# Kernel optimization log

Hardware: AMD Instinct MI355X
Metric: run time of the kernel (lower is better)

The kernel has to match this reference:

```python
import jax, jax.numpy as jnp
import numpy as np

B, L, C = 2, 2048, 1024
H, DK = 16, 64  # multiNum, dk
EPS = 1e-5
MASK_VAL = -2**15 + 1  # matches masked_fill value in torch source


def layer_norm(x, g, b):
    mu = jnp.mean(x, axis=-1, keepdims=True)
    var = jnp.var(x, axis=-1, keepdims=True)
    return (x - mu) * jax.lax.rsqrt(var + EPS) * g + b


def setup_inputs() -> dict:
    key = jax.random.key(0)
    ks = jax.random.split(key, 12)
    s_in = 1.0 / np.sqrt(C)
    s_attn = 1.0 / np.sqrt(H * DK)
    return {
        "qx": jax.random.normal(ks[0], (B, L, C), jnp.float32),
        "kx": jax.random.normal(ks[1], (B, L, C), jnp.float32),
        "vx": jax.random.normal(ks[2], (B, L, C), jnp.float32),
        "maskPAD": jax.random.randint(ks[3], (B, L, L), 0, 2, jnp.int32),
        "ln_g": jnp.ones((C,), jnp.float32),
        "ln_b": jnp.zeros((C,), jnp.float32),
        "wq": jax.random.uniform(ks[4], (C, H * DK), jnp.float32, -s_in, s_in),
        "bq": jax.random.uniform(ks[5], (H * DK,), jnp.float32, -s_in, s_in),
        "wk": jax.random.uniform(ks[6], (C, H * DK), jnp.float32, -s_in, s_in),
        "bk": jax.random.uniform(ks[7], (H * DK,), jnp.float32, -s_in, s_in),
        "wv": jax.random.uniform(ks[8], (C, H * DK), jnp.float32, -s_in, s_in),
        "bv": jax.random.uniform(ks[9], (H * DK,), jnp.float32, -s_in, s_in),
        "wo": jax.random.uniform(ks[10], (H * DK, C), jnp.float32, -s_attn, s_attn),
        "bo": jax.random.uniform(ks[11], (C,), jnp.float32, -s_attn, s_attn),
    }


def reference(qx, kx, vx, maskPAD, ln_g, ln_b, wq, bq, wk, bk, wv, bv, wo, bo):
    # PreLN with shared LayerNorm params across q/k/v (as in source)
    qn = layer_norm(qx, ln_g, ln_b)
    kn = layer_norm(kx, ln_g, ln_b)
    vn = layer_norm(vx, ln_g, ln_b)
    # project and split heads: [B, H, L, DK]
    q = (qn @ wq + bq).reshape(B, L, H, DK).transpose(0, 2, 1, 3)
    k = (kn @ wk + bk).reshape(B, L, H, DK).transpose(0, 2, 1, 3)
    v = (vn @ wv + bv).reshape(B, L, H, DK).transpose(0, 2, 1, 3)
    scores = jnp.einsum("bhqd,bhkd->bhqk", q, k) / np.sqrt(DK).astype(np.float32)
    scores = jnp.where((maskPAD == 0)[:, None, :, :], jnp.float32(MASK_VAL), scores)
    alpha = jax.nn.softmax(scores, axis=-1)
    z = jnp.einsum("bhqk,bhkd->bhqd", alpha, v)
    z = z.transpose(0, 2, 1, 3).reshape(B, L, H * DK)
    return z @ wo + bo
```

## Files before the change

kernel.cpp:

```cpp
#include <hip/hip_runtime.h>
#include <hip/hip_bf16.h>

#define B_ 2
#define L_ 2048
#define C_ 1024
#define H_ 16
#define DK_ 64
#define M_ (B_*L_)
#define MASK_VALF (-32767.0f)
#define LOG2E 1.44269504088896f

typedef __attribute__((ext_vector_type(8))) short bf16x8;
typedef __attribute__((ext_vector_type(4))) float f32x4;
typedef __attribute__((ext_vector_type(4))) unsigned uint4v;

static __device__ __forceinline__ short f2bf(float f) {
    __hip_bfloat16 h = __float2bfloat16(f);
    return *reinterpret_cast<short*>(&h);
}

static __device__ __forceinline__ float exp2_raw(float x) {
    float r;
    asm("v_exp_f32 %0, %1" : "=v"(r) : "v"(x));
    return r;
}
static __device__ __forceinline__ unsigned cvt_pk_bf16(float lo, float hi) {
    unsigned r;
    asm("v_cvt_pk_bf16_f32 %0, %1, %2" : "=v"(r) : "v"(lo), "v"(hi));
    return r;
}

__global__ __launch_bounds__(256) void prep_kernel(
    const float* __restrict__ qx, const float* __restrict__ kx, const float* __restrict__ vx,
    const float* __restrict__ g, const float* __restrict__ bias,
    short* __restrict__ qn, short* __restrict__ kn, short* __restrict__ vn,
    const float* __restrict__ wq, const float* __restrict__ wk,
    const float* __restrict__ wv, const float* __restrict__ wo,
    short* __restrict__ wqt, short* __restrict__ wkt,
    short* __restrict__ wvt, short* __restrict__ wot,
    const int* __restrict__ mask, unsigned long long* __restrict__ bits)
{
    const int bid = blockIdx.x;
    const int t = threadIdx.x;

    if (bid < 3*M_) {
        const int row = bid & (M_ - 1);
        const int which = bid >> 12;
        const float* src = (which == 0) ? qx : (which == 1) ? kx : vx;
        short* dst = (which == 0) ? qn : (which == 1) ? kn : vn;
        src += (size_t)row * C_;
        dst += (size_t)row * C_;
        float4 xv = reinterpret_cast<const float4*>(src)[t];
        float s  = xv.x + xv.y + xv.z + xv.w;
        float s2 = xv.x*xv.x + xv.y*xv.y + xv.z*xv.z + xv.w*xv.w;
        #pragma unroll
        for (int off = 32; off > 0; off >>= 1) {
            s  += __shfl_down(s, off);
            s2 += __shfl_down(s2, off);
        }
        __shared__ float red[8];
        const int wid = t >> 6, lane = t & 63;
        if (lane == 0) { red[wid] = s; red[4 + wid] = s2; }
        __syncthreads();
        const float ts  = red[0] + red[1] + red[2] + red[3];
        const float ts2 = red[4] + red[5] + red[6] + red[7];
        const float mu  = ts * (1.0f / C_);
        const float var = ts2 * (1.0f / C_) - mu * mu;
        const float rs  = rsqrtf(var + 1e-5f);
        float4 gv = reinterpret_cast<const float4*>(g)[t];
        float4 bv = reinterpret_cast<const float4*>(bias)[t];
        short4 o;
        o.x = f2bf((xv.x - mu) * rs * gv.x + bv.x);
        o.y = f2bf((xv.y - mu) * rs * gv.y + bv.y);
        o.z = f2bf((xv.z - mu) * rs * gv.z + bv.z);
        o.w = f2bf((xv.w - mu) * rs * gv.w + bv.w);
        reinterpret_cast<short4*>(dst)[t] = o;
    } else if (bid < 3*M_ + 4096) {
        const int b2 = bid - 3*M_;
        const int mz = b2 >> 10;
        const int bx = b2 & 31, by = (b2 >> 5) & 31;
        const float* w = (mz==0)?wq:(mz==1)?wk:(mz==2)?wv:wo;
        short* wt = (mz==0)?wqt:(mz==1)?wkt:(mz==2)?wvt:wot;
        __shared__ float tile[32][33];
        const int tx = t & 31, ty = t >> 5;
        const int k0 = bx * 32, n0 = by * 32;
        #pragma unroll
        for (int r = 0; r < 4; r++) {
            const int k = k0 + ty + r*8;
            tile[ty + r*8][tx] = w[(size_t)k * 1024 + n0 + tx];
        }
        __syncthreads();
        #pragma unroll
        for (int r = 0; r < 4; r++) {
            const int n = n0 + ty + r*8;
            wt[(size_t)n * 1024 + k0 + tx] = f2bf(tile[tx][ty + r*8]);
        }
    } else {
        const int b3 = bid - (3*M_ + 4096);
        const int gw = b3 * 4 + (t >> 6);
        const int lane = t & 63;
        const int k = (gw & 31) * 64 + lane;
        const int rowq = gw >> 5;
        const int v = mask[(size_t)rowq * L_ + k];
        unsigned long long bal = __ballot(v != 0);
        if (lane == 0) bits[gw] = bal;
    }
}

__device__ __forceinline__ void gemm_core_128(
    const short* __restrict__ Abf, const short* __restrict__ Bt,
    int m0, int n0, short* lds, f32x4 (&acc)[4][4])
{
    const int t = threadIdx.x, w = t >> 6, l = t & 63;
    const int wm = w >> 1, wn = w & 1;
    const int l15 = l & 15, l4 = l >> 4;
    const int srow = t >> 2, scol = (t & 3) * 8;
    const short* aS = Abf + (size_t)(m0 + srow) * 1024 + scol;
    const short* bS = Bt  + (size_t)(n0 + srow) * 1024 + scol;
    char* lb = (char*)lds;
    const int wb = w * 1024;

    #define GSTAGE(buf, kt) do {                                                   \
        const int ko = (kt) * 32;                                                  \
        char* dst = lb + (buf)*16384;                                              \
        __builtin_amdgcn_global_load_lds(                                          \
            (const __attribute__((address_space(1))) void*)(aS + ko),              \
            (__attribute__((address_space(3))) void*)(dst + wb), 16, 0, 0);        \
        __builtin_amdgcn_global_load_lds(                                          \
            (const __attribute__((address_space(1))) void*)(aS + 64*1024 + ko),    \
            (__attribute__((address_space(3))) void*)(dst + wb + 4096), 16, 0, 0); \
        __builtin_amdgcn_global_load_lds(                                          \
            (const __attribute__((address_space(1))) void*)(bS + ko),              \
            (__attribute__((address_space(3))) void*)(dst + 8192 + wb), 16, 0, 0); \
        __builtin_amdgcn_global_load_lds(                                          \
            (const __attribute__((address_space(1))) void*)(bS + 64*1024 + ko),    \
            (__attribute__((address_space(3))) void*)(dst + 8192 + wb + 4096), 16, 0, 0); \
    } while (0)

    GSTAGE(0, 0);
    for (int kt = 0; kt < 32; ++kt) {
        __syncthreads();
        if (kt + 1 < 32) GSTAGE((kt + 1) & 1, kt + 1);
        const short* Lb = lds + (kt & 1) * 8192;
        bf16x8 af[4], bfr[4];
        #pragma unroll
        for (int fm = 0; fm < 4; fm++)
            af[fm] = *reinterpret_cast<const bf16x8*>(&Lb[(wm*64 + fm*16 + l15)*32 + l4*8]);
        #pragma unroll
        for (int fn = 0; fn < 4; fn++)
            bfr[fn] = *reinterpret_cast<const bf16x8*>(&Lb[4096 + (wn*64 + fn*16 + l15)*32 + l4*8]);
        #pragma unroll
        for (int fm = 0; fm < 4; fm++)
            #pragma unroll
            for (int fn = 0; fn < 4; fn++)
                acc[fm][fn] = __builtin_amdgcn_mfma_f32_16x16x32_bf16(af[fm], bfr[fn], acc[fm][fn], 0, 0, 0);
    }
    #undef GSTAGE
}

__global__ __launch_bounds__(256) void gemm_proj(
    const short* __restrict__ qn, const short* __restrict__ kn, const short* __restrict__ vn,
    const short* __restrict__ wqt, const short* __restrict__ wkt, const short* __restrict__ wvt,
    const float* __restrict__ bq, const float* __restrict__ bk, const float* __restrict__ bv,
    short* __restrict__ qb, short* __restrict__ kb, short* __restrict__ vtb)
{
    const int pi = blockIdx.y;
    const short* Abf = (pi==0)?qn:(pi==1)?kn:vn;
    const short* Bt  = (pi==0)?wqt:(pi==1)?wkt:wvt;
    const float* bias= (pi==0)?bq:(pi==1)?bk:bv;
    short* outp      = (pi==0)?qb:(pi==1)?kb:vtb;
    const float scale = (pi==0)?(0.125f*LOG2E):1.0f;

    __shared__ short lds[16384];
    const int bx0 = blockIdx.x;
    const int bx = (bx0 & 7) * 32 + (bx0 >> 3);
    const int m0 = (bx >> 3) * 128, n0 = (bx & 7) * 128;
    f32x4 acc[4][4] = {};
    gemm_core_128(Abf, Bt, m0, n0, lds, acc);

    const int t = threadIdx.x, w = t >> 6, l = t & 63;
    const int wm = w >> 1, wn = w & 1, l15 = l & 15, l4 = l >> 4;
    #pragma unroll
    for (int fn = 0; fn < 4; fn++) {
        const int col = n0 + wn*64 + fn*16 + l15;
        const float bsv = bias[col];
        const int h = col >> 6, dk = col & 63;
        #pragma unroll
        for (int fm = 0; fm < 4; fm++) {
            const int row0 = m0 + wm*64 + fm*16 + l4*4;
            const int bb = row0 >> 11, lr0 = row0 & (L_ - 1);
            if (pi == 2) {
                const int lrp = (lr0 & ~63) | ((fm >> 1)*32 + l4*8 + (fm & 1)*4);
                short4 s4;
                #pragma unroll
                for (int r = 0; r < 4; r++)
                    ((short*)&s4)[r] = f2bf(acc[fm][fn][r] + bsv);
                *reinterpret_cast<short4*>(
                    &outp[(((size_t)bb*H_ + h)*DK_ + dk)*L_ + lrp]) = s4;
            } else {
                #pragma unroll
                for (int r = 0; r < 4; r++) {
                    const float vvf = (acc[fm][fn][r] + bsv) * scale;
                    outp[(((size_t)bb*H_ + h)*L_ + lr0 + r)*DK_ + dk] = f2bf(vvf);
                }
            }
        }
    }
}

__global__ __launch_bounds__(256) void gemm_out_k(
    const short* __restrict__ zb, const short* __restrict__ wot,
    const float* __restrict__ bo, float* __restrict__ out)
{
    __shared__ short lds[12288];
    const int t = threadIdx.x, w = t >> 6, l = t & 63;
    const int wm = w >> 1, wn = w & 1;
    const int l15 = l & 15, l4 = l >> 4;
    const int bx0 = blockIdx.x;
    const int bx = (bx0 & 7) * 64 + (bx0 >> 3);
    const int m0 = (bx >> 3) * 64, n0 = (bx & 7) * 128;

    const int srow = l >> 2, scol = (l & 3) * 8;
    const short* aS = zb  + (size_t)(m0 + w*16 + srow) * 1024 + scol;
    const short* bS = wot + (size_t)(n0 + w*32 + srow) * 1024 + scol;
    char* lb = (char*)lds;

    f32x4 acc[2][4] = {};

    #define OSTAGE(buf, kt) do {                                                    \
        const int ko = (kt) * 32;                                                   \
        char* dst = lb + (buf)*12288;                                               \
        __builtin_amdgcn_global_load_lds(                                           \
            (const __attribute__((address_space(1))) void*)(aS + ko),               \
            (__attribute__((address_space(3))) void*)(dst + w*1024), 16, 0, 0);     \
        __builtin_amdgcn_global_load_lds(                                           \
            (const __attribute__((address_space(1))) void*)(bS + ko),               \
            (__attribute__((address_space(3))) void*)(dst + 4096 + w*2048), 16, 0, 0); \
        __builtin_amdgcn_global_load_lds(                                           \
            (const __attribute__((address_space(1))) void*)(bS + 16*1024 + ko),     \
            (__attribute__((address_space(3))) void*)(dst + 4096 + w*2048 + 1024), 16, 0, 0); \
    } while (0)

    OSTAGE(0, 0);
    for (int kt = 0; kt < 32; ++kt) {
        __syncthreads();
        if (kt + 1 < 32) OSTAGE((kt + 1) & 1, kt + 1);
        const short* Lb = lds + (kt & 1) * 6144;
        bf16x8 af[2], bfr[4];
        #pragma unroll
        for (int fm = 0; fm < 2; fm++)
            af[fm] = *reinterpret_cast<const bf16x8*>(&Lb[(wm*32 + fm*16 + l15)*32 + l4*8]);
        #pragma unroll
        for (int fn = 0; fn < 4; fn++)
            bfr[fn] = *reinterpret_cast<const bf16x8*>(&Lb[2048 + (wn*64 + fn*16 + l15)*32 + l4*8]);
        #pragma unroll
        for (int fm = 0; fm < 2; fm++)
            #pragma unroll
            for (int fn = 0; fn < 4; fn++)
                acc[fm][fn] = __builtin_amdgcn_mfma_f32_16x16x32_bf16(af[fm], bfr[fn], acc[fm][fn], 0, 0, 0);
    }
    #undef OSTAGE

    #pragma unroll
    for (int fn = 0; fn < 4; fn++) {
        const int col = n0 + wn*64 + fn*16 + l15;
        const float bsv = bo[col];
        #pragma unroll
        for (int fm = 0; fm < 2; fm++) {
            #pragma unroll
            for (int r = 0; r < 4; r++) {
                const int row = m0 + wm*32 + fm*16 + l4*4 + r;
                out[(size_t)row * C_ + col] = acc[fm][fn][r] + bsv;
            }
        }
    }
}

__global__ __launch_bounds__(512) void attn_kernel(
    const short* __restrict__ qbuf, const short* __restrict__ kbuf, const short* __restrict__ vt,
    const unsigned long long* __restrict__ mbits, short* __restrict__ zb)
{
    __shared__ char SM[65536];
    const int t = threadIdx.x, w = t >> 6, l = t & 63;
    const int l15 = l & 15, l4 = l >> 4;
    const int bid = blockIdx.x;
    const int bh = bid & 31, qb = bid >> 5;
    const int qt0 = qb * 128;
    const int b = bh >> 4, h = bh & 15;
    const size_t base  = (size_t)bh * L_ * DK_;
    const size_t vbase = (size_t)bh * DK_ * L_;

    const int q = qt0 + w*16 + l15;

    const int srow = w*8 + (l >> 3);
    const int scolb = ((l & 7) * 16) ^ ((srow & 7) << 4);

    const char* gk = (const char*)(kbuf + base + (size_t)srow*DK_) + scolb;
    const char* gv = (const char*)(vt + vbase + (size_t)srow*L_) + scolb;

    const int sw = (l15 & 7) << 4;
    const char* pa = SM + l15*128 + ((l4*16) ^ sw);
    const char* pb = SM + l15*128 + ((64 + l4*16) ^ sw);
    const int l4s = l4 * 4;

    bf16x8 qf[2];
    #pragma unroll
    for (int kk = 0; kk < 2; kk++)
        qf[kk] = *reinterpret_cast<const bf16x8*>(&qbuf[base + (size_t)q*DK_ + kk*32 + l4*8]);

    const uint4* mq4 = reinterpret_cast<const uint4*>(mbits + ((size_t)b*L_ + q) * (L_/64));

    f32x4 oacc[4];
    #pragma unroll
    for (int nt = 0; nt < 4; nt++) oacc[nt] = (f32x4){0.f, 0.f, 0.f, 0.f};
    f32x4 lacc = (f32x4){0.f, 0.f, 0.f, 0.f};

    uint4v onesu = {0x3F803F80u, 0x3F803F80u, 0x3F803F80u, 0x3F803F80u};
    const bf16x8 onesv = *reinterpret_cast<const bf16x8*>(&onesu);

    #define STAGE2(DB) do {                                                          \
        __builtin_amdgcn_global_load_lds(                                            \
            (const __attribute__((address_space(1))) void*)(gk),                     \
            (__attribute__((address_space(3))) void*)(SM + (DB) + w*1024), 16, 0, 0); \
        __builtin_amdgcn_global_load_lds(                                            \
            (const __attribute__((address_space(1))) void*)(gv),                     \
            (__attribute__((address_space(3))) void*)(SM + (DB) + 8192 + w*1024), 16, 0, 0); \
        __builtin_amdgcn_global_load_lds(                                            \
            (const __attribute__((address_space(1))) void*)(gk + 8192),              \
            (__attribute__((address_space(3))) void*)(SM + (DB) + 16384 + w*1024), 16, 0, 0); \
        __builtin_amdgcn_global_load_lds(                                            \
            (const __attribute__((address_space(1))) void*)(gv + 128),               \
            (__attribute__((address_space(3))) void*)(SM + (DB) + 24576 + w*1024), 16, 0, 0); \
        gk += 16384; gv += 256;                                                      \
    } while (0)

    #define BODY(BOFF, mlo, mhi) do {                                               \
        f32x4 sfr[4];                                                                \
        __builtin_amdgcn_s_setprio(1);                                               \
        _Pragma("unroll")                                                            \
        for (int ct = 0; ct < 4; ct++) {                                             \
            bf16x8 kf0 = *reinterpret_cast<const bf16x8*>(pa + (BOFF) + ct*2048);    \
            bf16x8 kf1 = *reinterpret_cast<const bf16x8*>(pb + (BOFF) + ct*2048);    \
            f32x4 a = (f32x4){0.f, 0.f, 0.f, 0.f};                                   \
            a = __builtin_amdgcn_mfma_f32_16x16x32_bf16(kf0, qf[0], a, 0, 0, 0);     \
            a = __builtin_amdgcn_mfma_f32_16x16x32_bf16(kf1, qf[1], a, 0, 0, 0);     \
            sfr[ct] = a;                                                             \
        }                                                                            \
        __builtin_amdgcn_s_setprio(0);                                               \
        const unsigned msl = (mlo) >> l4s;                                           \
        const unsigned msh = (mhi) >> l4s;                                           \
        unsigned pu[8];                                                              \
        _Pragma("unroll")                                                            \
        for (int ct = 0; ct < 4; ct++) {                                             \
            const unsigned ms = (ct < 2) ? msl : msh;                                \
            const unsigned bp = (ct & 1) * 16;                                       \
            float p0 = exp2_raw((ms & (1u << (bp + 0))) ? sfr[ct][0] : MASK_VALF);   \
            float p1 = exp2_raw((ms & (1u << (bp + 1))) ? sfr[ct][1] : MASK_VALF);   \
            float p2 = exp2_raw((ms & (1u << (bp + 2))) ? sfr[ct][2] : MASK_VALF);   \
            float p3 = exp2_raw((ms & (1u << (bp + 3))) ? sfr[ct][3] : MASK_VALF);   \
            pu[ct*2]     = cvt_pk_bf16(p0, p1);                                      \
            pu[ct*2 + 1] = cvt_pk_bf16(p2, p3);                                      \
        }                                                                            \
        uint4v a0v = {pu[0], pu[1], pu[2], pu[3]};                                   \
        uint4v a1v = {pu[4], pu[5], pu[6], pu[7]};                                   \
        const bf16x8 af0 = *reinterpret_cast<const bf16x8*>(&a0v);                   \
        const bf16x8 af1 = *reinterpret_cast<const bf16x8*>(&a1v);                   \
        __builtin_amdgcn_s_setprio(1);                                               \
        lacc = __builtin_amdgcn_mfma_f32_16x16x32_bf16(af0, onesv, lacc, 0, 0, 0);   \
        lacc = __builtin_amdgcn_mfma_f32_16x16x32_bf16(af1, onesv, lacc, 0, 0, 0);   \
        _Pragma("unroll")                                                            \
        for (int nt = 0; nt < 4; nt++) {                                             \
            bf16x8 vf0 = *reinterpret_cast<const bf16x8*>(pa + (BOFF) + 8192 + nt*2048); \
            bf16x8 vf1 = *reinterpret_cast<const bf16x8*>(pb + (BOFF) + 8192 + nt*2048); \
            oacc[nt] = __builtin_amdgcn_mfma_f32_16x16x32_bf16(af0, vf0, oacc[nt], 0, 0, 0); \
            oacc[nt] = __builtin_amdgcn_mfma_f32_16x16x32_bf16(af1, vf1, oacc[nt], 0, 0, 0); \
        }                                                                            \
        __builtin_amdgcn_s_setprio(0);                                               \
    } while (0)

    STAGE2(0);
    uint4 mq = mq4[0], mqn;

    for (int it = 0; it < 16; ++it) {
        const int DB  = (it & 1) * 32768;
        const int DBn = ((it + 1) & 1) * 32768;
        __syncthreads();
        if (it + 1 < 16) { STAGE2(DBn); mqn = mq4[it + 1]; }
        BODY(DB,         mq.x, mq.y);
        BODY(DB + 16384, mq.z, mq.w);
        mq = mqn;
    }
    #undef STAGE2
    #undef BODY

    #pragma unroll
    for (int nt = 0; nt < 4; nt++) {
        #pragma unroll
        for (int r = 0; r < 4; r++) {
            const int qg = qt0 + w*16 + l4*4 + r;
            const float ov = oacc[nt][r] / lacc[r];
            zb[((size_t)b*L_ + qg)*C_ + h*DK_ + nt*16 + l15] = f2bf(ov);
        }
    }
}

extern "C" void kernel_launch(void* const* d_in, const int* in_sizes, int n_in,
                              void* d_out, int out_size, void* d_ws, size_t ws_size,
                              hipStream_t stream)
{
    (void)in_sizes; (void)n_in; (void)out_size; (void)ws_size;
    const float* qx = (const float*)d_in[0];
    const float* kx = (const float*)d_in[1];
    const float* vx = (const float*)d_in[2];
    const int*   mp = (const int*)d_in[3];
    const float* lg = (const float*)d_in[4];
    const float* lbt= (const float*)d_in[5];
    const float* wq = (const float*)d_in[6];
    const float* bq = (const float*)d_in[7];
    const float* wk = (const float*)d_in[8];
    const float* bk = (const float*)d_in[9];
    const float* wv = (const float*)d_in[10];
    const float* bv = (const float*)d_in[11];
    const float* wo = (const float*)d_in[12];
    const float* bo = (const float*)d_in[13];
    float* out = (float*)d_out;

    short* ws0 = (short*)d_ws;
    short* qn  = ws0;
    short* kn  = qn + (size_t)M_*C_;
    short* vn  = kn + (size_t)M_*C_;
    short* wqt = vn + (size_t)M_*C_;
    short* wkt = wqt + 1024*1024;
    short* wvt = wkt + 1024*1024;
    short* wot = wvt + 1024*1024;
    short* qbuf = wot + 1024*1024;
    short* kbuf = qbuf + (size_t)M_*C_;
    short* vtb  = kbuf + (size_t)M_*C_;
    short* zbuf = vtb + (size_t)M_*C_;
    unsigned long long* mbits = (unsigned long long*)(zbuf + (size_t)M_*C_);

    hipLaunchKernelGGL(prep_kernel, dim3(3*M_ + 4096 + (B_*L_*L_/64)/4), dim3(256), 0, stream,
                       qx, kx, vx, lg, lbt, qn, kn, vn,
                       wq, wk, wv, wo, wqt, wkt, wvt, wot, mp, mbits);
    hipLaunchKernelGGL(gemm_proj, dim3(256, 3), dim3(256), 0, stream,
                       qn, kn, vn, wqt, wkt, wvt, bq, bk, bv, qbuf, kbuf, vtb);
    hipLaunchKernelGGL(attn_kernel, dim3(512), dim3(512), 0, stream,
                       qbuf, kbuf, vtb, mbits, zbuf);
    hipLaunchKernelGGL(gemm_out_k, dim3(512), dim3(256), 0, stream,
                       zbuf, wot, bo, out);
}
```

Baseline: 131.6 us.

## Split attention key tiles across wave halves, each wave handling two query groups

Each wave now processes 32 query rows (two 16-row groups) against half of every staged key/value tile, instead of 16 rows against the whole tile. The two wave halves split the key dimension, and their partial outputs and row sums are combined through shared memory at the end. This reuses each K/V fragment loaded from LDS across two query groups, roughly halving LDS read traffic per MFMA, at the cost of more registers, an extra reduction pass with two barriers, and a launch_bounds occupancy hint.

```diff
diff --git a/kernel.cpp b/kernel.cpp
--- a/kernel.cpp
+++ b/kernel.cpp
@@ -276,13 +276,14 @@
     }
 }
 
-__global__ __launch_bounds__(512) void attn_kernel(
+__global__ __launch_bounds__(512, 4) void attn_kernel(
     const short* __restrict__ qbuf, const short* __restrict__ kbuf, const short* __restrict__ vt,
     const unsigned long long* __restrict__ mbits, short* __restrict__ zb)
 {
     __shared__ char SM[65536];
     const int t = threadIdx.x, w = t >> 6, l = t & 63;
     const int l15 = l & 15, l4 = l >> 4;
+    const int qslot = w & 3, par = w >> 2;
     const int bid = blockIdx.x;
     const int bh = bid & 31, qb = bid >> 5;
     const int qt0 = qb * 128;
@@ -290,11 +291,8 @@
     const size_t base  = (size_t)bh * L_ * DK_;
     const size_t vbase = (size_t)bh * DK_ * L_;
 
-    const int q = qt0 + w*16 + l15;
-
     const int srow = w*8 + (l >> 3);
     const int scolb = ((l & 7) * 16) ^ ((srow & 7) << 4);
-
     const char* gk = (const char*)(kbuf + base + (size_t)srow*DK_) + scolb;
     const char* gv = (const char*)(vt + vbase + (size_t)srow*L_) + scolb;
 
@@ -303,17 +301,29 @@
     const char* pb = SM + l15*128 + ((64 + l4*16) ^ sw);
     const int l4s = l4 * 4;
 
-    bf16x8 qf[2];
+    bf16x8 qf[2][2];
     #pragma unroll
-    for (int kk = 0; kk < 2; kk++)
-        qf[kk] = *reinterpret_cast<const bf16x8*>(&qbuf[base + (size_t)q*DK_ + kk*32 + l4*8]);
-
-    const uint4* mq4 = reinterpret_cast<const uint4*>(mbits + ((size_t)b*L_ + q) * (L_/64));
-
-    f32x4 oacc[4];
+    for (int g = 0; g < 2; g++) {
+        const int qr = qt0 + qslot*32 + g*16 + l15;
+        #pragma unroll
+        for (int kk = 0; kk < 2; kk++)
+            qf[g][kk] = *reinterpret_cast<const bf16x8*>(
+                &qbuf[base + (size_t)qr*DK_ + kk*32 + l4*8]);
+    }
+
+    const uint4* mbA = reinterpret_cast<const uint4*>(
+        mbits + ((size_t)b*L_ + qt0 + qslot*32 + l15) * (L_/64));
+    const uint4* mbB = reinterpret_cast<const uint4*>(
+        mbits + ((size_t)b*L_ + qt0 + qslot*32 + 16 + l15) * (L_/64));
+
+    f32x4 oacc[2][4];
     #pragma unroll
-    for (int nt = 0; nt < 4; nt++) oacc[nt] = (f32x4){0.f, 0.f, 0.f, 0.f};
-    f32x4 lacc = (f32x4){0.f, 0.f, 0.f, 0.f};
+    for (int g = 0; g < 2; g++)
+        #pragma unroll
+        for (int nt = 0; nt < 4; nt++) oacc[g][nt] = (f32x4){0.f, 0.f, 0.f, 0.f};
+    f32x4 lacc[2];
+    lacc[0] = (f32x4){0.f, 0.f, 0.f, 0.f};
+    lacc[1] = (f32x4){0.f, 0.f, 0.f, 0.f};
 
     uint4v onesu = {0x3F803F80u, 0x3F803F80u, 0x3F803F80u, 0x3F803F80u};
     const bf16x8 onesv = *reinterpret_cast<const bf16x8*>(&onesu);
@@ -334,72 +344,109 @@
         gk += 16384; gv += 256;                                                      \
     } while (0)
 
-    #define BODY(BOFF, mlo, mhi) do {                                               \
-        f32x4 sfr[4];                                                                \
+    #define BODY(BOFF, mAlo, mAhi, mBlo, mBhi) do {                                  \
+        f32x4 sfr[2][4];                                                             \
         __builtin_amdgcn_s_setprio(1);                                               \
         _Pragma("unroll")                                                            \
         for (int ct = 0; ct < 4; ct++) {                                             \
             bf16x8 kf0 = *reinterpret_cast<const bf16x8*>(pa + (BOFF) + ct*2048);    \
             bf16x8 kf1 = *reinterpret_cast<const bf16x8*>(pb + (BOFF) + ct*2048);    \
-            f32x4 a = (f32x4){0.f, 0.f, 0.f, 0.f};                                   \
-            a = __builtin_amdgcn_mfma_f32_16x16x32_bf16(kf0, qf[0], a, 0, 0, 0);     \
-            a = __builtin_amdgcn_mfma_f32_16x16x32_bf16(kf1, qf[1], a, 0, 0, 0);     \
-            sfr[ct] = a;                                                             \
+            f32x4 a0 = (f32x4){0.f, 0.f, 0.f, 0.f};                                  \
+            a0 = __builtin_amdgcn_mfma_f32_16x16x32_bf16(kf0, qf[0][0], a0, 0, 0, 0); \
+            a0 = __builtin_amdgcn_mfma_f32_16x16x32_bf16(kf1, qf[0][1], a0, 0, 0, 0); \
+            sfr[0][ct] = a0;                                                         \
+            f32x4 a1 = (f32x4){0.f, 0.f, 0.f, 0.f};                                  \
+            a1 = __builtin_amdgcn_mfma_f32_16x16x32_bf16(kf0, qf[1][0], a1, 0, 0, 0); \
+            a1 = __builtin_amdgcn_mfma_f32_16x16x32_bf16(kf1, qf[1][1], a1, 0, 0, 0); \
+            sfr[1][ct] = a1;                                                         \
         }                                                                            \
         __builtin_amdgcn_s_setprio(0);                                               \
-        const unsigned msl = (mlo) >> l4s;                                           \
-        const unsigned msh = (mhi) >> l4s;                                           \
-        unsigned pu[8];                                                              \
+        bf16x8 af0g[2], af1g[2];                                                     \
         _Pragma("unroll")                                                            \
-        for (int ct = 0; ct < 4; ct++) {                                             \
-            const unsigned ms = (ct < 2) ? msl : msh;                                \
-            const unsigned bp = (ct & 1) * 16;                                       \
-            float p0 = exp2_raw((ms & (1u << (bp + 0))) ? sfr[ct][0] : MASK_VALF);   \
-            float p1 = exp2_raw((ms & (1u << (bp + 1))) ? sfr[ct][1] : MASK_VALF);   \
-            float p2 = exp2_raw((ms & (1u << (bp + 2))) ? sfr[ct][2] : MASK_VALF);   \
-            float p3 = exp2_raw((ms & (1u << (bp + 3))) ? sfr[ct][3] : MASK_VALF);   \
-            pu[ct*2]     = cvt_pk_bf16(p0, p1);                                      \
-            pu[ct*2 + 1] = cvt_pk_bf16(p2, p3);                                      \
+        for (int g = 0; g < 2; g++) {                                                \
+            const unsigned msl = (g ? (mBlo) : (mAlo)) >> l4s;                       \
+            const unsigned msh = (g ? (mBhi) : (mAhi)) >> l4s;                       \
+            unsigned pu[8];                                                          \
+            _Pragma("unroll")                                                        \
+            for (int ct = 0; ct < 4; ct++) {                                         \
+                const unsigned ms = (ct < 2) ? msl : msh;                            \
+                const unsigned bp = (ct & 1) * 16;                                   \
+                float p0 = exp2_raw((ms & (1u << (bp + 0))) ? sfr[g][ct][0] : MASK_VALF); \
+                float p1 = exp2_raw((ms & (1u << (bp + 1))) ? sfr[g][ct][1] : MASK_VALF); \
+                float p2 = exp2_raw((ms & (1u << (bp + 2))) ? sfr[g][ct][2] : MASK_VALF); \
+                float p3 = exp2_raw((ms & (1u << (bp + 3))) ? sfr[g][ct][3] : MASK_VALF); \
+                pu[ct*2]     = cvt_pk_bf16(p0, p1);                                  \
+                pu[ct*2 + 1] = cvt_pk_bf16(p2, p3);                                  \
+            }                                                                        \
+            uint4v a0v = {pu[0], pu[1], pu[2], pu[3]};                               \
+            uint4v a1v = {pu[4], pu[5], pu[6], pu[7]};                               \
+            af0g[g] = *reinterpret_cast<const bf16x8*>(&a0v);                        \
+            af1g[g] = *reinterpret_cast<const bf16x8*>(&a1v);                        \
+            lacc[g] = __builtin_amdgcn_mfma_f32_16x16x32_bf16(af0g[g], onesv, lacc[g], 0, 0, 0); \
+            lacc[g] = __builtin_amdgcn_mfma_f32_16x16x32_bf16(af1g[g], onesv, lacc[g], 0, 0, 0); \
         }                                                                            \
-        uint4v a0v = {pu[0], pu[1], pu[2], pu[3]};                                   \
-        uint4v a1v = {pu[4], pu[5], pu[6], pu[7]};                                   \
-        const bf16x8 af0 = *reinterpret_cast<const bf16x8*>(&a0v);                   \
-        const bf16x8 af1 = *reinterpret_cast<const bf16x8*>(&a1v);                   \
         __builtin_amdgcn_s_setprio(1);                                               \
-        lacc = __builtin_amdgcn_mfma_f32_16x16x32_bf16(af0, onesv, lacc, 0, 0, 0);   \
-        lacc = __builtin_amdgcn_mfma_f32_16x16x32_bf16(af1, onesv, lacc, 0, 0, 0);   \
         _Pragma("unroll")                                                            \
         for (int nt = 0; nt < 4; nt++) {                                             \
             bf16x8 vf0 = *reinterpret_cast<const bf16x8*>(pa + (BOFF) + 8192 + nt*2048); \
             bf16x8 vf1 = *reinterpret_cast<const bf16x8*>(pb + (BOFF) + 8192 + nt*2048); \
-            oacc[nt] = __builtin_amdgcn_mfma_f32_16x16x32_bf16(af0, vf0, oacc[nt], 0, 0, 0); \
-            oacc[nt] = __builtin_amdgcn_mfma_f32_16x16x32_bf16(af1, vf1, oacc[nt], 0, 0, 0); \
+            oacc[0][nt] = __builtin_amdgcn_mfma_f32_16x16x32_bf16(af0g[0], vf0, oacc[0][nt], 0, 0, 0); \
+            oacc[0][nt] = __builtin_amdgcn_mfma_f32_16x16x32_bf16(af1g[0], vf1, oacc[0][nt], 0, 0, 0); \
+            oacc[1][nt] = __builtin_amdgcn_mfma_f32_16x16x32_bf16(af0g[1], vf0, oacc[1][nt], 0, 0, 0); \
+            oacc[1][nt] = __builtin_amdgcn_mfma_f32_16x16x32_bf16(af1g[1], vf1, oacc[1][nt], 0, 0, 0); \
         }                                                                            \
         __builtin_amdgcn_s_setprio(0);                                               \
     } while (0)
 
     STAGE2(0);
-    uint4 mq = mq4[0], mqn;
+    uint4 mqA = mbA[0], mqB = mbB[0], mqAn, mqBn;
+    const int poff = par * 16384;
 
     for (int it = 0; it < 16; ++it) {
         const int DB  = (it & 1) * 32768;
         const int DBn = ((it + 1) & 1) * 32768;
         __syncthreads();
-        if (it + 1 < 16) { STAGE2(DBn); mqn = mq4[it + 1]; }
-        BODY(DB,         mq.x, mq.y);
-        BODY(DB + 16384, mq.z, mq.w);
-        mq = mqn;
+        if (it + 1 < 16) { STAGE2(DBn); mqAn = mbA[it + 1]; mqBn = mbB[it + 1]; }
+        if (par == 0) BODY(DB + poff, mqA.x, mqA.y, mqB.x, mqB.y);
+        else          BODY(DB + poff, mqA.z, mqA.w, mqB.z, mqB.w);
+        mqA = mqAn; mqB = mqBn;
     }
     #undef STAGE2
     #undef BODY
 
-    #pragma unroll
-    for (int nt = 0; nt < 4; nt++) {
-        #pragma unroll
-        for (int r = 0; r < 4; r++) {
-            const int qg = qt0 + w*16 + l4*4 + r;
-            const float ov = oacc[nt][r] / lacc[r];
-            zb[((size_t)b*L_ + qg)*C_ + h*DK_ + nt*16 + l15] = f2bf(ov);
+    __syncthreads();
+    if (par == 1) {
+        float* dst = (float*)(SM + ((size_t)(qslot*64 + l) * 176));
+        #pragma unroll
+        for (int g = 0; g < 2; g++)
+            #pragma unroll
+            for (int nt = 0; nt < 4; nt++)
+                *reinterpret_cast<f32x4*>(dst + g*16 + nt*4) = oacc[g][nt];
+        *reinterpret_cast<f32x4*>(dst + 32) = lacc[0];
+        *reinterpret_cast<f32x4*>(dst + 36) = lacc[1];
+    }
+    __syncthreads();
+    if (par == 0) {
+        const float* src = (const float*)(SM + ((size_t)(qslot*64 + l) * 176));
+        #pragma unroll
+        for (int g = 0; g < 2; g++)
+            #pragma unroll
+            for (int nt = 0; nt < 4; nt++)
+                oacc[g][nt] += *reinterpret_cast<const f32x4*>(src + g*16 + nt*4);
+        lacc[0] += *reinterpret_cast<const f32x4*>(src + 32);
+        lacc[1] += *reinterpret_cast<const f32x4*>(src + 36);
+
+        #pragma unroll
+        for (int g = 0; g < 2; g++) {
+            #pragma unroll
+            for (int nt = 0; nt < 4; nt++) {
+                #pragma unroll
+                for (int r = 0; r < 4; r++) {
+                    const int qg = qt0 + qslot*32 + g*16 + l4*4 + r;
+                    const float ov = oacc[g][nt][r] / lacc[g][r];
+                    zb[((size_t)b*L_ + qg)*C_ + h*DK_ + nt*16 + l15] = f2bf(ov);
+                }
+            }
         }
     }
 }
```

Result: no change. 132.7 us (+0.9%).
